# Kernel tuning notes

Hardware: AMD Instinct MI355X
Metric: run time of the kernel (lower is better)

## Reference

```python
import jax, jax.numpy as jnp
import numpy as np

EPS = 1e-6  # F.pairwise_distance default eps, added to the difference


def setup_inputs() -> dict:
    key = jax.random.key(0)
    k1, k2 = jax.random.split(key)
    N, NS, NQ, D = 2048, 5, 8, 256
    x = jax.random.normal(k1, (N, NS + NQ, D), dtype=jnp.float32)
    label = jax.random.randint(k2, (N,), 0, N, dtype=jnp.int64)
    return {"x": x, "label": label, "n_s": NS, "n_q": NQ}


def reference(x, label, n_s, n_q):
    # x: [N, n_s+n_q, D]
    anchors = jnp.mean(x[:, :n_s, :], axis=1)               # [N, D] prototypes
    N, D = anchors.shape
    queries = x[:, n_s:n_s + n_q, :].reshape(N * n_q, D)     # [N*n_q, D]

    # Exact ||q - a + eps||^2 via GEMM expansion (matches F.pairwise_distance(.,.)**2):
    # ||q-a||^2 + 2*eps*sum(q-a) + D*eps^2
    q_sq = jnp.sum(queries * queries, axis=-1)               # [N*n_q]
    a_sq = jnp.sum(anchors * anchors, axis=-1)               # [N]
    cross = queries @ anchors.T                              # [N*n_q, N]
    q_sum = jnp.sum(queries, axis=-1)                        # [N*n_q]
    a_sum = jnp.sum(anchors, axis=-1)                        # [N]
    dist_sq = (q_sq[:, None] + a_sq[None, :] - 2.0 * cross
               + 2.0 * EPS * (q_sum[:, None] - a_sum[None, :])
               + D * EPS * EPS)
    logits = -dist_sq                                        # [N*n_q, N]

    lab = jnp.repeat(label, n_q)                             # [N*n_q]
    logp = jax.nn.log_softmax(logits, axis=-1)
    nloss = -jnp.mean(jnp.take_along_axis(logp, lab[:, None], axis=1))
    prec1 = jnp.mean((jnp.argmax(logits, axis=-1) == lab).astype(jnp.float32)) * 100.0
    return nloss, prec1
```

## Files before the change

### kernel.cpp

```cpp
#include <hip/hip_runtime.h>
#include <math.h>

#define EPS  1e-6f
#define DD   256
#define NSUP 5
#define NQ   8
#define SEQ  13
#define L2E  1.44269504088896f
#define LN2  0.693147180559945f
#define NEP  2048
#define NROW 16384
#define NCOL 2048

typedef short bf16x8 __attribute__((ext_vector_type(8)));
typedef unsigned short u16x4 __attribute__((ext_vector_type(4)));
typedef float f32x4  __attribute__((ext_vector_type(4)));

__device__ __forceinline__ ushort f2bf(float f) {
  union { float f; unsigned u; } v; v.f = f;
  unsigned r = v.u + 0x7FFFu + ((v.u >> 16) & 1u);
  return (ushort)(r >> 16);
}
__device__ __forceinline__ float bf2f(short u) {
  union { unsigned u; float f; } v; v.u = ((unsigned)(unsigned short)u) << 16;
  return v.f;
}

__global__ __launch_bounds__(256) void proto_prep(
    const float* __restrict__ x, float* __restrict__ cb,
    ushort* __restrict__ Asw, ushort* __restrict__ Qsw,
    float* __restrict__ accum, int* __restrict__ fincount) {
  const int tid = threadIdx.x, g = tid >> 6, l = tid & 63;
  const int n = blockIdx.x * 4 + g;
  if (blockIdx.x == 0 && tid == 0) { accum[0] = 0.f; accum[1] = 0.f; fincount[0] = 0; }

  const float4* xr4 = (const float4*)(x + (size_t)n * SEQ * DD);

  const int d0   = l * 4;
  const int kk   = d0 >> 5, quad = (d0 >> 3) & 3, j = d0 & 7;
  const size_t chunk_d = (size_t)kk * 64 + (size_t)quad * 16;

  float4 a = {0.f, 0.f, 0.f, 0.f};
  #pragma unroll
  for (int s = 0; s < NSUP; ++s) {
    float4 v = xr4[s * 64 + l];
    a.x += v.x; a.y += v.y; a.z += v.z; a.w += v.w;
  }
  a.x *= 0.2f; a.y *= 0.2f; a.z *= 0.2f; a.w *= 0.2f;
  {
    const size_t idx = (((size_t)(n >> 4) * 8) * 64 + chunk_d + (n & 15)) * 8 + j;
    u16x4 o = {f2bf(a.x), f2bf(a.y), f2bf(a.z), f2bf(a.w)};
    *(u16x4*)(Asw + idx) = o;
  }
  float s1 = a.x + a.y + a.z + a.w;
  float s2 = a.x * a.x + a.y * a.y + a.z * a.z + a.w * a.w;
  #pragma unroll
  for (int off = 32; off; off >>= 1) {
    s1 += __shfl_xor(s1, off);
    s2 += __shfl_xor(s2, off);
  }
  if (l == 0) cb[n] = -L2E * (s2 - 2.f * EPS * s1);

  #pragma unroll
  for (int s = 0; s < NQ; ++s) {
    float4 q = xr4[(NSUP + s) * 64 + l];
    const int row = n * NQ + s;
    const size_t idx = (((size_t)(row >> 4) * 8) * 64 + chunk_d + (row & 15)) * 8 + j;
    u16x4 o = {f2bf(q.x), f2bf(q.y), f2bf(q.z), f2bf(q.w)};
    *(u16x4*)(Qsw + idx) = o;
  }
}

__global__ __launch_bounds__(256, 2) void proto_main(
    const ushort* __restrict__ Qsw, const ushort* __restrict__ Asw,
    const float* __restrict__ cb, const int* __restrict__ label,
    float* __restrict__ accum, int* __restrict__ fincount,
    float* __restrict__ out) {
  const int tid  = threadIdx.x;
  const int wid  = tid >> 6, lane = tid & 63;
  const int quad = lane >> 4, lcol = lane & 15;
  const int r0   = blockIdx.x * 32;

  __shared__ __align__(16) ushort smem[4][2][4096];
  __shared__ float scb[4][512];
  __shared__ float sm[4][32], ssh[4][32], slab[32];
  __shared__ int   sbi[4][32];

  const bf16x8* qb = (const bf16x8*)Qsw;
  const bf16x8* bb = (const bf16x8*)Asw;
  const int T0 = wid * 32;

  #pragma unroll
  for (int i = 0; i < 8; ++i)
    scb[wid][i * 64 + lane] = cb[T0 * 16 + i * 64 + lane];

  bf16x8 af[2][8];
  #pragma unroll
  for (int set = 0; set < 2; ++set) {
    const size_t base = ((size_t)((r0 >> 4) + set) * 8) * 64 + lane;
    #pragma unroll
    for (int kk = 0; kk < 8; ++kk) af[set][kk] = qb[base + (size_t)kk * 64];
  }

  float m[2][4], s[2][4];
  int   bi[2][4];
  #pragma unroll
  for (int set = 0; set < 2; ++set)
    #pragma unroll
    for (int i = 0; i < 4; ++i) {
      m[set][i] = -1e30f; s[set][i] = 0.f; bi[set][i] = 0x7fffffff;
    }

  auto dma_tile = [&](int T, int bufi) {
    const ushort* src = Asw + ((size_t)T * 8) * 512 + (size_t)lane * 8;
    #pragma unroll
    for (int kk = 0; kk < 8; ++kk)
      __builtin_amdgcn_global_load_lds(
          (const __attribute__((address_space(1))) void*)(src + kk * 512),
          (__attribute__((address_space(3))) void*)(&smem[wid][bufi][kk * 512]),
          16, 0, 0);
  };

  dma_tile(T0, 0);

  #pragma unroll 1
  for (int t = 0; t < 32; ++t) {
    const int Tn = (t + 1 < 32) ? T0 + t + 1 : T0 + t;
    dma_tile(Tn, (t + 1) & 1);
    __builtin_amdgcn_s_waitcnt(0xF78);
    __builtin_amdgcn_sched_barrier(0);

    const ushort* B = &smem[wid][t & 1][0];
    f32x4 c0 = {0.f, 0.f, 0.f, 0.f}, c1 = {0.f, 0.f, 0.f, 0.f};
    #pragma unroll
    for (int kk = 0; kk < 8; ++kk) {
      bf16x8 b = *(const bf16x8*)(B + kk * 512 + lane * 8);
      c0 = __builtin_amdgcn_mfma_f32_16x16x32_bf16(af[0][kk], b, c0, 0, 0, 0);
      c1 = __builtin_amdgcn_mfma_f32_16x16x32_bf16(af[1][kk], b, c1, 0, 0, 0);
    }
    const int   colIdx = (T0 + t) * 16 + lcol;
    const float cbv    = scb[wid][t * 16 + lcol];
    #pragma unroll
    for (int set = 0; set < 2; ++set) {
      #pragma unroll
      for (int i = 0; i < 4; ++i) {
        float cv = (set == 0) ? c0[i] : c1[i];
        float v2 = fmaf(cv, 2.f * L2E, cbv);
        float dv = v2 - m[set][i];
        bool  gt = dv > 0.f;
        float e  = exp2f(-fabsf(dv));
        s[set][i]  = fmaf(s[set][i], gt ? e : 1.f, gt ? 1.f : e);
        m[set][i]  = fmaxf(m[set][i], v2);
        bi[set][i] = gt ? colIdx : bi[set][i];
      }
    }
  }

  #pragma unroll
  for (int mask = 1; mask < 16; mask <<= 1) {
    #pragma unroll
    for (int set = 0; set < 2; ++set)
      #pragma unroll
      for (int i = 0; i < 4; ++i) {
        float om = __shfl_xor(m[set][i], mask);
        float os = __shfl_xor(s[set][i], mask);
        int   oi = __shfl_xor(bi[set][i], mask);
        float nm = fmaxf(m[set][i], om);
        s[set][i] = s[set][i] * exp2f(m[set][i] - nm) + os * exp2f(om - nm);
        bool better = (om > m[set][i]) || (om == m[set][i] && oi < bi[set][i]);
        bi[set][i] = better ? oi : bi[set][i];
        m[set][i]  = nm;
      }
  }

  if (lcol == 0) {
    #pragma unroll
    for (int set = 0; set < 2; ++set)
      #pragma unroll
      for (int i = 0; i < 4; ++i) {
        int rl = set * 16 + quad * 4 + i;
        sm[wid][rl] = m[set][i]; ssh[wid][rl] = s[set][i]; sbi[wid][rl] = bi[set][i];
      }
  }

  {
    const int r = tid >> 3, l = tid & 7;
    const int row = r0 + r;
    const int lab = label[row >> 3];
    const size_t qbase = ((size_t)(row >> 4) * 8 + l) * 64 + (row & 15);
    const size_t abase = ((size_t)(lab >> 4) * 8 + l) * 64 + (lab & 15);
    float dot = 0.f;
    #pragma unroll
    for (int q16 = 0; q16 < 4; ++q16) {
      bf16x8 qv = qb[qbase + (size_t)q16 * 16];
      bf16x8 av = bb[abase + (size_t)q16 * 16];
      #pragma unroll
      for (int j = 0; j < 8; ++j) dot = fmaf(bf2f(qv[j]), bf2f(av[j]), dot);
    }
    #pragma unroll
    for (int mask = 1; mask < 8; mask <<= 1) dot += __shfl_xor(dot, mask);
    if (l == 0) slab[r] = fmaf(dot, 2.f * L2E, cb[lab]);
  }
  __syncthreads();

  if (tid < 32) {
    float mm = sm[0][tid], sv = ssh[0][tid];
    int   b  = sbi[0][tid];
    #pragma unroll
    for (int w = 1; w < 4; ++w) {
      float om = sm[w][tid], os = ssh[w][tid];
      int   oi = sbi[w][tid];
      float nm = fmaxf(mm, om);
      sv = sv * exp2f(mm - nm) + os * exp2f(om - nm);
      bool better = (om > mm) || (om == mm && oi < b);
      b = better ? oi : b;
      mm = nm;
    }
    const int row = r0 + tid;
    const int lb  = label[row >> 3];
    float loss = LN2 * (mm + log2f(sv) - slab[tid]);
    float corr = (b == lb) ? 1.f : 0.f;
    #pragma unroll
    for (int mask = 16; mask; mask >>= 1) {
      loss += __shfl_xor(loss, mask);
      corr += __shfl_xor(corr, mask);
    }
    if (tid == 0) {
      atomicAdd(&accum[0], loss);
      atomicAdd(&accum[1], corr);
      __threadfence();
      if (atomicAdd(fincount, 1) == (int)gridDim.x - 1) {
        out[0] = atomicAdd(&accum[0], 0.f) / (float)NROW;
        out[1] = atomicAdd(&accum[1], 0.f) * 100.f / (float)NROW;
      }
    }
  }
}

extern "C" void kernel_launch(void* const* d_in, const int* in_sizes, int n_in,
                              void* d_out, int out_size, void* d_ws, size_t ws_size,
                              hipStream_t stream) {
  const float* x     = (const float*)d_in[0];
  const int*   label = (const int*)d_in[1];
  float* out = (float*)d_out;

  float*  W        = (float*)d_ws;
  float*  accum    = W;
  int*    fincount = (int*)(W + 2);
  float*  cb       = W + 16;
  ushort* Asw      = (ushort*)(cb + NCOL);
  ushort* Qsw      = Asw + (size_t)NCOL * DD;

  hipLaunchKernelGGL(proto_prep, dim3(NEP / 4), dim3(256), 0, stream,
                     x, cb, Asw, Qsw, accum, fincount);
  hipLaunchKernelGGL(proto_main, dim3(NROW / 32), dim3(256), 0, stream,
                     Qsw, Asw, cb, label, accum, fincount, out);
}
```

Baseline: 130.9 us.

## Share B tiles across waves and split columns across blocks with cross-block merge

The main kernel now gives each block 64 query rows and one quarter of the anchor columns. The four waves cooperatively DMA each shared B tile into LDS and sync with block barriers, where before each wave streamed its own private column range. Partial softmax/argmax states go to global scratch, and the last-arriving block for each row group (tracked by a counter) merges them and computes the loss. This cuts LDS traffic and the per-block register footprint and raises grid size, at the cost of extra global round-trips, atomics and a per-tile __syncthreads.

```diff
diff --git a/kernel.cpp b/kernel.cpp
--- a/kernel.cpp
+++ b/kernel.cpp
@@ -11,6 +11,8 @@
 #define NEP  2048
 #define NROW 16384
 #define NCOL 2048
+#define NRG  256
+#define NTB  32
 
 typedef short bf16x8 __attribute__((ext_vector_type(8)));
 typedef unsigned short u16x4 __attribute__((ext_vector_type(4)));
@@ -29,10 +31,12 @@
 __global__ __launch_bounds__(256) void proto_prep(
     const float* __restrict__ x, float* __restrict__ cb,
     ushort* __restrict__ Asw, ushort* __restrict__ Qsw,
-    float* __restrict__ accum, int* __restrict__ fincount) {
+    float* __restrict__ accum, int* __restrict__ fincount,
+    int* __restrict__ rgcount) {
   const int tid = threadIdx.x, g = tid >> 6, l = tid & 63;
   const int n = blockIdx.x * 4 + g;
   if (blockIdx.x == 0 && tid == 0) { accum[0] = 0.f; accum[1] = 0.f; fincount[0] = 0; }
+  if (tid == 0 && blockIdx.x < NRG) rgcount[blockIdx.x] = 0;
 
   const float4* xr4 = (const float4*)(x + (size_t)n * SEQ * DD);
 
@@ -71,157 +75,154 @@
   }
 }
 
-__global__ __launch_bounds__(256, 2) void proto_main(
+__global__ __launch_bounds__(256) void proto_main(
     const ushort* __restrict__ Qsw, const ushort* __restrict__ Asw,
     const float* __restrict__ cb, const int* __restrict__ label,
+    float* __restrict__ pm, float* __restrict__ ps, int* __restrict__ pb,
+    int* __restrict__ rgcount,
     float* __restrict__ accum, int* __restrict__ fincount,
     float* __restrict__ out) {
   const int tid  = threadIdx.x;
   const int wid  = tid >> 6, lane = tid & 63;
   const int quad = lane >> 4, lcol = lane & 15;
-  const int r0   = blockIdx.x * 32;
-
-  __shared__ __align__(16) ushort smem[4][2][4096];
-  __shared__ float scb[4][512];
-  __shared__ float sm[4][32], ssh[4][32], slab[32];
-  __shared__ int   sbi[4][32];
+  const int rg   = blockIdx.x >> 2;
+  const int qq   = blockIdx.x & 3;
+  const int r0   = rg * 64;
+  const int T0   = qq * NTB;
+
+  __shared__ __align__(16) ushort sB[2][4096];
+  __shared__ float slab[64];
+  __shared__ int   s_old;
 
   const bf16x8* qb = (const bf16x8*)Qsw;
   const bf16x8* bb = (const bf16x8*)Asw;
-  const int T0 = wid * 32;
-
-  #pragma unroll
-  for (int i = 0; i < 8; ++i)
-    scb[wid][i * 64 + lane] = cb[T0 * 16 + i * 64 + lane];
-
-  bf16x8 af[2][8];
-  #pragma unroll
-  for (int set = 0; set < 2; ++set) {
-    const size_t base = ((size_t)((r0 >> 4) + set) * 8) * 64 + lane;
-    #pragma unroll
-    for (int kk = 0; kk < 8; ++kk) af[set][kk] = qb[base + (size_t)kk * 64];
-  }
-
-  float m[2][4], s[2][4];
-  int   bi[2][4];
-  #pragma unroll
-  for (int set = 0; set < 2; ++set)
-    #pragma unroll
-    for (int i = 0; i < 4; ++i) {
-      m[set][i] = -1e30f; s[set][i] = 0.f; bi[set][i] = 0x7fffffff;
-    }
-
-  auto dma_tile = [&](int T, int bufi) {
-    const ushort* src = Asw + ((size_t)T * 8) * 512 + (size_t)lane * 8;
-    #pragma unroll
-    for (int kk = 0; kk < 8; ++kk)
+
+  bf16x8 af[8];
+  {
+    const size_t base = ((size_t)((r0 >> 4) + wid) * 8) * 64 + lane;
+    #pragma unroll
+    for (int kk = 0; kk < 8; ++kk) af[kk] = qb[base + (size_t)kk * 64];
+  }
+
+  float m[4], s[4];
+  int   bi[4];
+  #pragma unroll
+  for (int i = 0; i < 4; ++i) { m[i] = -1e30f; s[i] = 0.f; bi[i] = 0x7fffffff; }
+
+  auto dma = [&](int T, int bufi) {
+    #pragma unroll
+    for (int c = 0; c < 2; ++c) {
+      const int chunk = wid * 2 + c;
+      const ushort* src = Asw + ((size_t)T * 8 + chunk) * 512 + (size_t)lane * 8;
       __builtin_amdgcn_global_load_lds(
-          (const __attribute__((address_space(1))) void*)(src + kk * 512),
-          (__attribute__((address_space(3))) void*)(&smem[wid][bufi][kk * 512]),
+          (const __attribute__((address_space(1))) void*)src,
+          (__attribute__((address_space(3))) void*)(&sB[bufi][chunk * 512]),
           16, 0, 0);
+    }
   };
 
-  dma_tile(T0, 0);
+  dma(T0, 0);
+  __syncthreads();
 
   #pragma unroll 1
-  for (int t = 0; t < 32; ++t) {
-    const int Tn = (t + 1 < 32) ? T0 + t + 1 : T0 + t;
-    dma_tile(Tn, (t + 1) & 1);
-    __builtin_amdgcn_s_waitcnt(0xF78);
-    __builtin_amdgcn_sched_barrier(0);
-
-    const ushort* B = &smem[wid][t & 1][0];
-    f32x4 c0 = {0.f, 0.f, 0.f, 0.f}, c1 = {0.f, 0.f, 0.f, 0.f};
+  for (int t = 0; t < NTB; ++t) {
+    if (t + 1 < NTB) dma(T0 + t + 1, (t + 1) & 1);
+    const ushort* B = sB[t & 1];
+    f32x4 c0 = {0.f, 0.f, 0.f, 0.f};
     #pragma unroll
     for (int kk = 0; kk < 8; ++kk) {
       bf16x8 b = *(const bf16x8*)(B + kk * 512 + lane * 8);
-      c0 = __builtin_amdgcn_mfma_f32_16x16x32_bf16(af[0][kk], b, c0, 0, 0, 0);
-      c1 = __builtin_amdgcn_mfma_f32_16x16x32_bf16(af[1][kk], b, c1, 0, 0, 0);
+      c0 = __builtin_amdgcn_mfma_f32_16x16x32_bf16(af[kk], b, c0, 0, 0, 0);
     }
     const int   colIdx = (T0 + t) * 16 + lcol;
-    const float cbv    = scb[wid][t * 16 + lcol];
-    #pragma unroll
-    for (int set = 0; set < 2; ++set) {
+    const float cbv    = cb[colIdx];
+    #pragma unroll
+    for (int i = 0; i < 4; ++i) {
+      float v2 = fmaf(c0[i], 2.f * L2E, cbv);
+      float dv = v2 - m[i];
+      bool  gt = dv > 0.f;
+      float e  = exp2f(-fabsf(dv));
+      s[i]  = fmaf(s[i], gt ? e : 1.f, gt ? 1.f : e);
+      m[i]  = fmaxf(m[i], v2);
+      bi[i] = gt ? colIdx : bi[i];
+    }
+    __syncthreads();
+  }
+
+  #pragma unroll
+  for (int mask = 1; mask < 16; mask <<= 1) {
+    #pragma unroll
+    for (int i = 0; i < 4; ++i) {
+      float om = __shfl_xor(m[i], mask);
+      float os = __shfl_xor(s[i], mask);
+      int   oi = __shfl_xor(bi[i], mask);
+      float nm = fmaxf(m[i], om);
+      s[i] = s[i] * exp2f(m[i] - nm) + os * exp2f(om - nm);
+      bool better = (om > m[i]) || (om == m[i] && oi < bi[i]);
+      bi[i] = better ? oi : bi[i];
+      m[i]  = nm;
+    }
+  }
+
+  if (lcol == 0) {
+    #pragma unroll
+    for (int i = 0; i < 4; ++i) {
+      const int row = r0 + wid * 16 + quad * 4 + i;
+      atomicExch(&pm[qq * NROW + row], m[i]);
+      atomicExch(&ps[qq * NROW + row], s[i]);
+      atomicExch(&pb[qq * NROW + row], bi[i]);
+    }
+    __threadfence();
+  }
+  __syncthreads();
+  if (tid == 0) s_old = atomicAdd(&rgcount[rg], 1);
+  __syncthreads();
+  if (s_old != 3) return;
+
+  {
+    const int rl = tid >> 2, l = tid & 3;
+    const int row = r0 + rl;
+    const int lab = label[row >> 3];
+    float dot = 0.f;
+    #pragma unroll
+    for (int c = 0; c < 2; ++c) {
+      const int kk = l * 2 + c;
+      const size_t qc = ((size_t)(row >> 4) * 8 + kk) * 64 + (row & 15);
+      const size_t ac = ((size_t)(lab >> 4) * 8 + kk) * 64 + (lab & 15);
       #pragma unroll
-      for (int i = 0; i < 4; ++i) {
-        float cv = (set == 0) ? c0[i] : c1[i];
-        float v2 = fmaf(cv, 2.f * L2E, cbv);
-        float dv = v2 - m[set][i];
-        bool  gt = dv > 0.f;
-        float e  = exp2f(-fabsf(dv));
-        s[set][i]  = fmaf(s[set][i], gt ? e : 1.f, gt ? 1.f : e);
-        m[set][i]  = fmaxf(m[set][i], v2);
-        bi[set][i] = gt ? colIdx : bi[set][i];
+      for (int qd = 0; qd < 4; ++qd) {
+        bf16x8 qv = qb[qc + qd * 16];
+        bf16x8 av = bb[ac + qd * 16];
+        #pragma unroll
+        for (int j = 0; j < 8; ++j) dot = fmaf(bf2f(qv[j]), bf2f(av[j]), dot);
       }
     }
-  }
-
-  #pragma unroll
-  for (int mask = 1; mask < 16; mask <<= 1) {
-    #pragma unroll
-    for (int set = 0; set < 2; ++set)
-      #pragma unroll
-      for (int i = 0; i < 4; ++i) {
-        float om = __shfl_xor(m[set][i], mask);
-        float os = __shfl_xor(s[set][i], mask);
-        int   oi = __shfl_xor(bi[set][i], mask);
-        float nm = fmaxf(m[set][i], om);
-        s[set][i] = s[set][i] * exp2f(m[set][i] - nm) + os * exp2f(om - nm);
-        bool better = (om > m[set][i]) || (om == m[set][i] && oi < bi[set][i]);
-        bi[set][i] = better ? oi : bi[set][i];
-        m[set][i]  = nm;
-      }
-  }
-
-  if (lcol == 0) {
-    #pragma unroll
-    for (int set = 0; set < 2; ++set)
-      #pragma unroll
-      for (int i = 0; i < 4; ++i) {
-        int rl = set * 16 + quad * 4 + i;
-        sm[wid][rl] = m[set][i]; ssh[wid][rl] = s[set][i]; sbi[wid][rl] = bi[set][i];
-      }
-  }
-
-  {
-    const int r = tid >> 3, l = tid & 7;
-    const int row = r0 + r;
-    const int lab = label[row >> 3];
-    const size_t qbase = ((size_t)(row >> 4) * 8 + l) * 64 + (row & 15);
-    const size_t abase = ((size_t)(lab >> 4) * 8 + l) * 64 + (lab & 15);
-    float dot = 0.f;
-    #pragma unroll
-    for (int q16 = 0; q16 < 4; ++q16) {
-      bf16x8 qv = qb[qbase + (size_t)q16 * 16];
-      bf16x8 av = bb[abase + (size_t)q16 * 16];
-      #pragma unroll
-      for (int j = 0; j < 8; ++j) dot = fmaf(bf2f(qv[j]), bf2f(av[j]), dot);
-    }
-    #pragma unroll
-    for (int mask = 1; mask < 8; mask <<= 1) dot += __shfl_xor(dot, mask);
-    if (l == 0) slab[r] = fmaf(dot, 2.f * L2E, cb[lab]);
-  }
-  __syncthreads();
-
-  if (tid < 32) {
-    float mm = sm[0][tid], sv = ssh[0][tid];
-    int   b  = sbi[0][tid];
-    #pragma unroll
-    for (int w = 1; w < 4; ++w) {
-      float om = sm[w][tid], os = ssh[w][tid];
-      int   oi = sbi[w][tid];
+    dot += __shfl_xor(dot, 1);
+    dot += __shfl_xor(dot, 2);
+    if (l == 0) slab[rl] = fmaf(dot, 2.f * L2E, cb[lab]);
+  }
+  __syncthreads();
+
+  if (tid < 64) {
+    const int row = r0 + tid;
+    float mm = -1e30f, sv = 0.f;
+    int   b  = 0x7fffffff;
+    #pragma unroll
+    for (int k = 0; k < 4; ++k) {
+      float om = atomicAdd(&pm[k * NROW + row], 0.f);
+      float os = atomicAdd(&ps[k * NROW + row], 0.f);
+      int   oi = atomicAdd(&pb[k * NROW + row], 0);
       float nm = fmaxf(mm, om);
       sv = sv * exp2f(mm - nm) + os * exp2f(om - nm);
       bool better = (om > mm) || (om == mm && oi < b);
       b = better ? oi : b;
       mm = nm;
     }
-    const int row = r0 + tid;
-    const int lb  = label[row >> 3];
+    const int lb = label[row >> 3];
     float loss = LN2 * (mm + log2f(sv) - slab[tid]);
     float corr = (b == lb) ? 1.f : 0.f;
     #pragma unroll
-    for (int mask = 16; mask; mask >>= 1) {
+    for (int mask = 32; mask; mask >>= 1) {
       loss += __shfl_xor(loss, mask);
       corr += __shfl_xor(corr, mask);
     }
@@ -229,7 +230,7 @@
       atomicAdd(&accum[0], loss);
       atomicAdd(&accum[1], corr);
       __threadfence();
-      if (atomicAdd(fincount, 1) == (int)gridDim.x - 1) {
+      if (atomicAdd(fincount, 1) == NRG - 1) {
         out[0] = atomicAdd(&accum[0], 0.f) / (float)NROW;
         out[1] = atomicAdd(&accum[1], 0.f) * 100.f / (float)NROW;
       }
@@ -247,12 +248,17 @@
   float*  W        = (float*)d_ws;
   float*  accum    = W;
   int*    fincount = (int*)(W + 2);
-  float*  cb       = W + 16;
-  ushort* Asw      = (ushort*)(cb + NCOL);
+  int*    rgcount  = (int*)(W + 16);
+  float*  cb       = W + 16 + NRG;
+  float*  pm       = cb + NCOL;
+  float*  ps       = pm + 4 * NROW;
+  int*    pb       = (int*)(ps + 4 * NROW);
+  ushort* Asw      = (ushort*)(pb + 4 * NROW);
   ushort* Qsw      = Asw + (size_t)NCOL * DD;
 
   hipLaunchKernelGGL(proto_prep, dim3(NEP / 4), dim3(256), 0, stream,
-                     x, cb, Asw, Qsw, accum, fincount);
-  hipLaunchKernelGGL(proto_main, dim3(NROW / 32), dim3(256), 0, stream,
-                     Qsw, Asw, cb, label, accum, fincount, out);
-}
+                     x, cb, Asw, Qsw, accum, fincount, rgcount);
+  hipLaunchKernelGGL(proto_main, dim3(NRG * 4), dim3(256), 0, stream,
+                     Qsw, Asw, cb, label, pm, ps, pb, rgcount,
+                     accum, fincount, out);
+}
```

Result: slower. 186.4 us (+42.4%).
